# Performance work log

Hardware: AMD Instinct MI355X
Metric: run time of the kernel (lower is better)

## Reference

```python
import jax, jax.numpy as jnp
import numpy as np

B, S, D = 8, 2048, 256


def setup_inputs() -> dict:
    key = jax.random.key(0)
    k1, k2, k3, k4, k5 = jax.random.split(key, 5)
    head = jax.random.normal(k1, (B, S, D), dtype=jnp.float32)
    dep = jax.random.normal(k2, (B, S, D), dtype=jnp.float32)
    edge_U = jax.random.normal(k3, (D, D), dtype=jnp.float32) / np.sqrt(D)
    edge_W = jax.random.normal(k4, (1, 2 * D), dtype=jnp.float32) / np.sqrt(2 * D)
    edge_b = jax.random.normal(k5, (1,), dtype=jnp.float32)
    return {"head": head, "dep": dep, "edge_U": edge_U, "edge_W": edge_W, "edge_b": edge_b}


def reference(head, dep, edge_U, edge_W, edge_b):
    # t1[b,i,o] = head[b,i,:] @ U @ dep[b,o,:]  -> [B,S,S]
    t1 = jnp.einsum('bid,de,boe->bio', head, edge_U, dep)
    # t2: linear over pairwise concat(head_i, dep_o); decomposes into two
    # broadcast-added matvecs (same math as W @ concat, no [B,S^2,2D] tensor).
    d = head.shape[-1]
    wh, wd = edge_W[0, :d], edge_W[0, d:]
    hs = head @ wh  # [B,S]
    ds = dep @ wd   # [B,S]
    t2 = hs[:, :, None] + ds[:, None, :]  # [B,S,S]
    return t1 + t2 + edge_b[0]
```

## Files before the change

kernel.cpp:

```cpp
#include <hip/hip_runtime.h>
#include <hip/hip_bf16.h>
#include <stdint.h>
#include <stddef.h>

#define B_ 8
#define S_ 2048
#define D_ 256
#define NROWS (B_ * S_)

typedef __attribute__((ext_vector_type(8))) short short8;
typedef __attribute__((ext_vector_type(4))) short short4v;
typedef __attribute__((ext_vector_type(4))) float f32x4;

__device__ __forceinline__ short bf16of(float f) {
  union { float f; unsigned u; } x; x.f = f;
  unsigned r = x.u + 0x7FFFu + ((x.u >> 16) & 1u);
  return (short)(r >> 16);
}

__device__ __forceinline__ void async_ld16(const void* g, void* s) {
  __builtin_amdgcn_global_load_lds(
      (const __attribute__((address_space(1))) void*)g,
      (__attribute__((address_space(3))) void*)s, 16, 0, 0);
}

__global__ void k_prep_u(const float* __restrict__ U, short* __restrict__ UT) {
  int n = blockIdx.x;
  int k = threadIdx.x;
  UT[n * D_ + k] = bf16of(U[k * D_ + n]);
}

__global__ void k_rows(const float* __restrict__ head, const float* __restrict__ dep,
                       const float* __restrict__ W,
                       float* __restrict__ hs, float* __restrict__ ds,
                       short* __restrict__ headB, short* __restrict__ depB) {
  const float* X; const float* wv; float* sv; short* XB;
  if (blockIdx.y == 0) { X = head; wv = W;      sv = hs; XB = headB; }
  else                 { X = dep;  wv = W + D_; sv = ds; XB = depB;  }
  const int row = blockIdx.x * 4 + (threadIdx.x >> 6);
  const int l = threadIdx.x & 63;
  const float4 v  = *(const float4*)(X + (size_t)row * D_ + l * 4);
  const float4 wq = *(const float4*)(wv + l * 4);
  short4v pk;
  pk[0] = bf16of(v.x); pk[1] = bf16of(v.y); pk[2] = bf16of(v.z); pk[3] = bf16of(v.w);
  *(short4v*)(XB + (size_t)row * D_ + l * 4) = pk;
  float p = v.x * wq.x + v.y * wq.y + v.z * wq.z + v.w * wq.w;
  p += __shfl_xor(p, 1); p += __shfl_xor(p, 2); p += __shfl_xor(p, 4);
  p += __shfl_xor(p, 8); p += __shfl_xor(p, 16); p += __shfl_xor(p, 32);
  if (l == 0) sv[row] = p;
}

__launch_bounds__(256, 2)
__global__ void k_ahat(const short* __restrict__ headB, const short* __restrict__ UT,
                       short* __restrict__ Ahat) {
  __shared__ __align__(16) short sU[4 * 128 * 32];
  __shared__ __align__(16) short sH[4 * 128 * 32];
  const int t = threadIdx.x;
  const int w = t >> 6;
  const int l = t & 63;
  const int quad = l >> 4;
  const int nbase = blockIdx.x * 128;
  const int mbase = blockIdx.y * 128;

  f32x4 acc[4][4];
#pragma unroll
  for (int i = 0; i < 4; ++i)
#pragma unroll
    for (int j = 0; j < 4; ++j) acc[i][j] = (f32x4)0.0f;

  for (int it = 0; it < 2; ++it) {
    __syncthreads();
#pragma unroll
    for (int kb = 0; kb < 4; ++kb) {
#pragma unroll
      for (int c = 0; c < 2; ++c) {
        int q = c * 256 + t;
        int r = q >> 2, qc = q & 3;
        int kk = it * 128 + kb * 32 + qc * 8;
        async_ld16(UT + (size_t)(nbase + r) * D_ + kk, (char*)sU + kb * 8192 + q * 16);
        async_ld16(headB + (size_t)(mbase + r) * D_ + kk, (char*)sH + kb * 8192 + q * 16);
      }
    }
    __syncthreads();
    const short8* pU = (const short8*)sU;
    const short8* pH = (const short8*)sH;
#pragma unroll
    for (int kb = 0; kb < 4; ++kb) {
      short8 aF[4], bF[4];
#pragma unroll
      for (int mt = 0; mt < 4; ++mt)
        aF[mt] = pU[(kb * 128 + (w >> 1) * 64 + mt * 16 + (l & 15)) * 4 + quad];
#pragma unroll
      for (int nt = 0; nt < 4; ++nt)
        bF[nt] = pH[(kb * 128 + (w & 1) * 64 + nt * 16 + (l & 15)) * 4 + quad];
#pragma unroll
      for (int mt = 0; mt < 4; ++mt)
#pragma unroll
        for (int nt = 0; nt < 4; ++nt)
          acc[mt][nt] = __builtin_amdgcn_mfma_f32_16x16x32_bf16(aF[mt], bF[nt], acc[mt][nt], 0, 0, 0);
    }
  }

#pragma unroll
  for (int mt = 0; mt < 4; ++mt) {
    int n_loc = (w >> 1) * 64 + mt * 16 + quad * 4;
#pragma unroll
    for (int nt = 0; nt < 4; ++nt) {
      int i_loc = (w & 1) * 64 + nt * 16 + (l & 15);
      short4v pk;
      pk[0] = bf16of(acc[mt][nt][0]); pk[1] = bf16of(acc[mt][nt][1]);
      pk[2] = bf16of(acc[mt][nt][2]); pk[3] = bf16of(acc[mt][nt][3]);
      *(short4v*)(Ahat + (size_t)(mbase + i_loc) * D_ + nbase + n_loc) = pk;
    }
  }
}

__launch_bounds__(256, 3)
__global__ void k_main(const short* __restrict__ Ahat, const short* __restrict__ depB,
                       const float* __restrict__ hs, const float* __restrict__ ds,
                       const float* __restrict__ eb, float* __restrict__ out) {
  __shared__ __align__(16) short sA[2 * 128 * 32];
  __shared__ __align__(16) short sD[2 * 128 * 32];
  __shared__ float hs_s[128];
  __shared__ float ds_s[128];
  const int t = threadIdx.x;
  const int w = t >> 6;
  const int l = t & 63;
  const int quad = l >> 4;
  const int b = blockIdx.z;
  const int mbase = blockIdx.y * 128;
  const int nbase = blockIdx.x * 128;

  if (t < 128) hs_s[t] = hs[b * S_ + mbase + t];
  else         ds_s[t - 128] = ds[b * S_ + nbase + t - 128];

  f32x4 acc[4][4];
#pragma unroll
  for (int i = 0; i < 4; ++i)
#pragma unroll
    for (int j = 0; j < 4; ++j) acc[i][j] = (f32x4)0.0f;

  for (int it = 0; it < 4; ++it) {
    __syncthreads();
#pragma unroll
    for (int kb = 0; kb < 2; ++kb) {
#pragma unroll
      for (int c = 0; c < 2; ++c) {
        int q = c * 256 + t;
        int r = q >> 2, qc = q & 3;
        int kk = it * 64 + kb * 32 + qc * 8;
        async_ld16(Ahat + (size_t)(b * S_ + mbase + r) * D_ + kk, (char*)sA + kb * 8192 + q * 16);
        async_ld16(depB + (size_t)(b * S_ + nbase + r) * D_ + kk, (char*)sD + kb * 8192 + q * 16);
      }
    }
    __syncthreads();
    const short8* pA = (const short8*)sA;
    const short8* pD = (const short8*)sD;
#pragma unroll
    for (int kb = 0; kb < 2; ++kb) {
      short8 aF[4], bF[4];
#pragma unroll
      for (int mt = 0; mt < 4; ++mt)
        aF[mt] = pD[(kb * 128 + (w >> 1) * 64 + mt * 16 + (l & 15)) * 4 + quad];
#pragma unroll
      for (int nt = 0; nt < 4; ++nt)
        bF[nt] = pA[(kb * 128 + (w & 1) * 64 + nt * 16 + (l & 15)) * 4 + quad];
#pragma unroll
      for (int mt = 0; mt < 4; ++mt)
#pragma unroll
        for (int nt = 0; nt < 4; ++nt)
          acc[mt][nt] = __builtin_amdgcn_mfma_f32_16x16x32_bf16(aF[mt], bF[nt], acc[mt][nt], 0, 0, 0);
    }
  }

  const float bias = eb[0];
#pragma unroll
  for (int mt = 0; mt < 4; ++mt) {
    int o_loc = (w >> 1) * 64 + mt * 16 + quad * 4;
    float4 dsv = *(const float4*)&ds_s[o_loc];
#pragma unroll
    for (int nt = 0; nt < 4; ++nt) {
      int i_loc = (w & 1) * 64 + nt * 16 + (l & 15);
      float hv = hs_s[i_loc] + bias;
      f32x4 a = acc[mt][nt];
      float4 o4;
      o4.x = a[0] + hv + dsv.x;
      o4.y = a[1] + hv + dsv.y;
      o4.z = a[2] + hv + dsv.z;
      o4.w = a[3] + hv + dsv.w;
      *(float4*)(out + (size_t)(b * S_ + mbase + i_loc) * S_ + nbase + o_loc) = o4;
    }
  }
}

extern "C" void kernel_launch(void* const* d_in, const int* in_sizes, int n_in,
                              void* d_out, int out_size, void* d_ws, size_t ws_size,
                              hipStream_t stream) {
  const float* head = (const float*)d_in[0];
  const float* dep  = (const float*)d_in[1];
  const float* U    = (const float*)d_in[2];
  const float* W    = (const float*)d_in[3];
  const float* eb   = (const float*)d_in[4];
  float* out = (float*)d_out;

  char* ws = (char*)d_ws;
  short* UT    = (short*)ws;
  float* hs    = (float*)(ws + (128 << 10));
  float* ds    = (float*)(ws + (192 << 10));
  short* headB = (short*)(ws + (256 << 10));
  short* depB  = (short*)(ws + (256 << 10) + (8 << 20));
  short* Ahat  = (short*)(ws + (256 << 10) + (16 << 20));

  k_prep_u<<<dim3(256), dim3(256), 0, stream>>>(U, UT);
  k_rows<<<dim3(NROWS / 4, 2), dim3(256), 0, stream>>>(head, dep, W, hs, ds, headB, depB);
  k_ahat<<<dim3(2, 128), dim3(256), 0, stream>>>(headB, UT, Ahat);
  k_main<<<dim3(16, 16, 8), dim3(256), 0, stream>>>(Ahat, depB, hs, ds, eb, out);
}
```

Before: 191.2 us.

## Double-buffer main GEMM via register prefetch and merge prep kernels

```diff
diff --git a/kernel.cpp b/kernel.cpp
--- a/kernel.cpp
+++ b/kernel.cpp
@@ -24,30 +24,35 @@
       (__attribute__((address_space(3))) void*)s, 16, 0, 0);
 }
 
-__global__ void k_prep_u(const float* __restrict__ U, short* __restrict__ UT) {
-  int n = blockIdx.x;
-  int k = threadIdx.x;
-  UT[n * D_ + k] = bf16of(U[k * D_ + n]);
-}
-
-__global__ void k_rows(const float* __restrict__ head, const float* __restrict__ dep,
-                       const float* __restrict__ W,
-                       float* __restrict__ hs, float* __restrict__ ds,
-                       short* __restrict__ headB, short* __restrict__ depB) {
-  const float* X; const float* wv; float* sv; short* XB;
-  if (blockIdx.y == 0) { X = head; wv = W;      sv = hs; XB = headB; }
-  else                 { X = dep;  wv = W + D_; sv = ds; XB = depB;  }
-  const int row = blockIdx.x * 4 + (threadIdx.x >> 6);
-  const int l = threadIdx.x & 63;
-  const float4 v  = *(const float4*)(X + (size_t)row * D_ + l * 4);
-  const float4 wq = *(const float4*)(wv + l * 4);
-  short4v pk;
-  pk[0] = bf16of(v.x); pk[1] = bf16of(v.y); pk[2] = bf16of(v.z); pk[3] = bf16of(v.w);
-  *(short4v*)(XB + (size_t)row * D_ + l * 4) = pk;
-  float p = v.x * wq.x + v.y * wq.y + v.z * wq.z + v.w * wq.w;
-  p += __shfl_xor(p, 1); p += __shfl_xor(p, 2); p += __shfl_xor(p, 4);
-  p += __shfl_xor(p, 8); p += __shfl_xor(p, 16); p += __shfl_xor(p, 32);
-  if (l == 0) sv[row] = p;
+__global__ void k_pre(const float* __restrict__ head, const float* __restrict__ dep,
+                      const float* __restrict__ U, const float* __restrict__ W,
+                      float* __restrict__ hs, float* __restrict__ ds,
+                      short* __restrict__ headB, short* __restrict__ depB,
+                      short* __restrict__ UT) {
+  const int bid = blockIdx.x;
+  const int t = threadIdx.x;
+  if (bid < 8192) {
+    const float* X; const float* wv; float* sv; short* XB;
+    if (bid < 4096) { X = head; wv = W;      sv = hs; XB = headB; }
+    else            { X = dep;  wv = W + D_; sv = ds; XB = depB;  }
+    const int row = (bid & 4095) * 4 + (t >> 6);
+    const int l = t & 63;
+    const float4 v  = *(const float4*)(X + (size_t)row * D_ + l * 4);
+    const float4 wq = *(const float4*)(wv + l * 4);
+    short4v pk;
+    pk[0] = bf16of(v.x); pk[1] = bf16of(v.y); pk[2] = bf16of(v.z); pk[3] = bf16of(v.w);
+    *(short4v*)(XB + (size_t)row * D_ + l * 4) = pk;
+    float p = v.x * wq.x + v.y * wq.y + v.z * wq.z + v.w * wq.w;
+    p += __shfl_xor(p, 1); p += __shfl_xor(p, 2); p += __shfl_xor(p, 4);
+    p += __shfl_xor(p, 8); p += __shfl_xor(p, 16); p += __shfl_xor(p, 32);
+    if (l == 0) sv[row] = p;
+  } else {
+    const int k0 = (bid - 8192) * 4;
+    const int n = t;
+#pragma unroll
+    for (int kk = 0; kk < 4; ++kk)
+      UT[n * D_ + k0 + kk] = bf16of(U[(k0 + kk) * D_ + n]);
+  }
 }
 
 __launch_bounds__(256, 2)
@@ -115,12 +120,12 @@
   }
 }
 
-__launch_bounds__(256, 3)
+__launch_bounds__(256, 2)
 __global__ void k_main(const short* __restrict__ Ahat, const short* __restrict__ depB,
                        const float* __restrict__ hs, const float* __restrict__ ds,
                        const float* __restrict__ eb, float* __restrict__ out) {
-  __shared__ __align__(16) short sA[2 * 128 * 32];
-  __shared__ __align__(16) short sD[2 * 128 * 32];
+  __shared__ __align__(16) short sA[2][2 * 128 * 32];
+  __shared__ __align__(16) short sD[2][2 * 128 * 32];
   __shared__ float hs_s[128];
   __shared__ float ds_s[128];
   const int t = threadIdx.x;
@@ -140,22 +145,37 @@
 #pragma unroll
     for (int j = 0; j < 4; ++j) acc[i][j] = (f32x4)0.0f;
 
+  const int row0 = t >> 3;
+  const int half = (t >> 2) & 1;
+  const int part = t & 3;
+  const short* gA = Ahat + (size_t)(b * S_ + mbase) * D_ + half * 32 + part * 8;
+  const short* gD = depB + (size_t)(b * S_ + nbase) * D_ + half * 32 + part * 8;
+  const int ldsOff = half * 4096 + row0 * 32 + part * 8;
+
+  float4 rA[4], rD[4];
+#pragma unroll
+  for (int c = 0; c < 4; ++c) {
+    rA[c] = *(const float4*)(gA + (size_t)(row0 + 32 * c) * D_);
+    rD[c] = *(const float4*)(gD + (size_t)(row0 + 32 * c) * D_);
+  }
+#pragma unroll
+  for (int c = 0; c < 4; ++c) {
+    *(float4*)((char*)&sA[0][0] + (ldsOff + c * 1024) * 2) = rA[c];
+    *(float4*)((char*)&sD[0][0] + (ldsOff + c * 1024) * 2) = rD[c];
+  }
+  __syncthreads();
+
   for (int it = 0; it < 4; ++it) {
-    __syncthreads();
-#pragma unroll
-    for (int kb = 0; kb < 2; ++kb) {
-#pragma unroll
-      for (int c = 0; c < 2; ++c) {
-        int q = c * 256 + t;
-        int r = q >> 2, qc = q & 3;
-        int kk = it * 64 + kb * 32 + qc * 8;
-        async_ld16(Ahat + (size_t)(b * S_ + mbase + r) * D_ + kk, (char*)sA + kb * 8192 + q * 16);
-        async_ld16(depB + (size_t)(b * S_ + nbase + r) * D_ + kk, (char*)sD + kb * 8192 + q * 16);
+    const int p = it & 1;
+    if (it < 3) {
+#pragma unroll
+      for (int c = 0; c < 4; ++c) {
+        rA[c] = *(const float4*)(gA + (size_t)(row0 + 32 * c) * D_ + (it + 1) * 64);
+        rD[c] = *(const float4*)(gD + (size_t)(row0 + 32 * c) * D_ + (it + 1) * 64);
       }
     }
-    __syncthreads();
-    const short8* pA = (const short8*)sA;
-    const short8* pD = (const short8*)sD;
+    const short8* pA = (const short8*)sA[p];
+    const short8* pD = (const short8*)sD[p];
 #pragma unroll
     for (int kb = 0; kb < 2; ++kb) {
       short8 aF[4], bF[4];
@@ -170,6 +190,14 @@
 #pragma unroll
         for (int nt = 0; nt < 4; ++nt)
           acc[mt][nt] = __builtin_amdgcn_mfma_f32_16x16x32_bf16(aF[mt], bF[nt], acc[mt][nt], 0, 0, 0);
+    }
+    if (it < 3) {
+#pragma unroll
+      for (int c = 0; c < 4; ++c) {
+        *(float4*)((char*)&sA[1 - p][0] + (ldsOff + c * 1024) * 2) = rA[c];
+        *(float4*)((char*)&sD[1 - p][0] + (ldsOff + c * 1024) * 2) = rD[c];
+      }
+      __syncthreads();
     }
   }
 
@@ -211,8 +239,7 @@
   short* depB  = (short*)(ws + (256 << 10) + (8 << 20));
   short* Ahat  = (short*)(ws + (256 << 10) + (16 << 20));
 
-  k_prep_u<<<dim3(256), dim3(256), 0, stream>>>(U, UT);
-  k_rows<<<dim3(NROWS / 4, 2), dim3(256), 0, stream>>>(head, dep, W, hs, ds, headB, depB);
+  k_pre<<<dim3(8256), dim3(256), 0, stream>>>(head, dep, U, W, hs, ds, headB, depB, UT);
   k_ahat<<<dim3(2, 128), dim3(256), 0, stream>>>(headB, UT, Ahat);
   k_main<<<dim3(16, 16, 8), dim3(256), 0, stream>>>(Ahat, depB, hs, ds, eb, out);
 }
```

After: 193.1 us. Within noise of the previous version (+1.0%).
